# Kernel tuning notes

Measured on AMD Instinct MI355X. Metric: run time of the kernel, lower is better.

Reference implementation:

```python
import jax, jax.numpy as jnp
import numpy as np

B, N, C = 4, 2048, 1024
H, D = 16, 64  # num_heads, head_dim; C = H*D
R = 16         # lora rank
SCALE = D ** -0.5


def setup_inputs() -> dict:
    key = jax.random.key(0)
    ks = jax.random.split(key, 6)
    return {
        "query": jax.random.normal(ks[0], (B, N, C), dtype=jnp.float32),
        "mask": jax.random.normal(ks[1], (B, 1, N, N), dtype=jnp.float32),
        "W_qkv": jax.random.normal(ks[2], (C, 3 * C), dtype=jnp.float32) * (C ** -0.5),
        "magnitude": jnp.ones((1, H, 1, 1), dtype=jnp.float32),
        "W_loraA": jax.random.normal(ks[3], (C, R), dtype=jnp.float32) * (C ** -0.5),
        "W_loraB": jax.random.normal(ks[4], (R, C), dtype=jnp.float32) * (R ** -0.5),
        "W_proj": jax.random.normal(ks[5], (C, C), dtype=jnp.float32) * (C ** -0.5),
    }


def reference(query, mask, W_qkv, magnitude, W_loraA, W_loraB, W_proj):
    # qkv projection: [B,N,3C] -> [3,B,H,N,D]
    qkv = (query @ W_qkv).reshape(B, N, 3, H, D).transpose(2, 0, 3, 1, 4)
    q, k, v = qkv[0], qkv[1], qkv[2]
    # LoRA/DoRA delta fused into q before attention
    delta = (query @ W_loraA) @ W_loraB                     # [B,N,C]
    delta = delta.reshape(B, N, H, D).transpose(0, 2, 1, 3)  # [B,H,N,D]
    q = q + magnitude * delta
    # attention
    attn = jnp.einsum('bhnd,bhmd->bhnm', q, k) * SCALE + mask
    attn = jax.nn.softmax(attn, axis=-1)
    out = jnp.einsum('bhnm,bhmd->bhnd', attn, v)            # [B,H,N,D]
    out = out.transpose(0, 2, 1, 3).reshape(B, N, C)
    return out @ W_proj
```

## Files before the change

kernel.cpp:

```cpp
#include <hip/hip_runtime.h>
#include <hip/hip_bf16.h>

#define Bd 4
#define Nd 2048
#define Cd 1024
#define Hd 16
#define Dd 64
#define Rd 16
#define KAUG 1056
#define SCALEf 0.125f
#define PIT 72

using short8 = __attribute__((ext_vector_type(8))) short;
using f32x4  = __attribute__((ext_vector_type(4))) float;

static __device__ __forceinline__ ushort f2bf(float f) {
    __hip_bfloat16 h = __float2bfloat16(f);
    return *reinterpret_cast<ushort*>(&h);
}

#define GLOAD_LDS16(g, l) __builtin_amdgcn_global_load_lds( \
    (const __attribute__((address_space(1))) void*)(g),      \
    (__attribute__((address_space(3))) void*)(l), 16, 0, 0)

__global__ __launch_bounds__(256) void pack_a_kernel(
    const float* __restrict__ query, ushort* __restrict__ Aaug)
{
    const int row = blockIdx.x;
    const int t = threadIdx.x;
    const float4 v = *(const float4*)&query[(size_t)row * Cd + t * 4];
    ushort4 u;
    u.x = f2bf(v.x); u.y = f2bf(v.y); u.z = f2bf(v.z); u.w = f2bf(v.w);
    *(ushort4*)&Aaug[(size_t)row * KAUG + t * 4] = u;
}

__global__ __launch_bounds__(256) void pack_wat_kernel(
    const float* __restrict__ WA, ushort* __restrict__ WAT)
{
    const int idx = blockIdx.x * 256 + threadIdx.x;
    const int c = idx >> 4, r = idx & 15;
    WAT[r * 1024 + c] = f2bf(WA[idx]);
}

__global__ __launch_bounds__(64) void lora_mfma_kernel(
    const ushort* __restrict__ Aro, const ushort* __restrict__ WAT,
    ushort* __restrict__ Awr)
{
    const int lane = threadIdx.x;
    const int quad = lane >> 4, lc = lane & 15;
    const int row0 = blockIdx.x * 16;
    f32x4 acc = {0.f, 0.f, 0.f, 0.f};
    #pragma unroll 4
    for (int k0 = 0; k0 < 1024; k0 += 32) {
        const short8 a = *(const short8*)&Aro[(size_t)(row0 + lc) * KAUG + k0 + quad * 8];
        const short8 b = *(const short8*)&WAT[lc * 1024 + k0 + quad * 8];
        acc = __builtin_amdgcn_mfma_f32_16x16x32_bf16(a, b, acc, 0, 0, 0);
    }
    #pragma unroll
    for (int ri = 0; ri < 4; ++ri) {
        const size_t row = row0 + quad * 4 + ri;
        Awr[row * KAUG + 1024 + lc] = f2bf(acc[ri]);
        Awr[row * KAUG + 1040 + lc] = 0;
    }
}

__global__ __launch_bounds__(256) void pack_bqkv_kernel(
    const float* __restrict__ Wqkv, const float* __restrict__ WloraB,
    const float* __restrict__ magnitude, ushort* __restrict__ BT)
{
    __shared__ float tile[32][33];
    const int k0 = blockIdx.x * 32, n0 = blockIdx.y * 32;
    const int tx = threadIdx.x & 31, ty = threadIdx.x >> 5;
    #pragma unroll
    for (int i = 0; i < 4; ++i) {
        const int k = k0 + ty + i * 8;
        const int n = n0 + tx;
        float v;
        if (k < 1024)                      v = Wqkv[(size_t)k * 3072 + n];
        else if (k < 1040 && n < 1024)     v = magnitude[n >> 6] * WloraB[(k - 1024) * Cd + n];
        else                               v = 0.f;
        tile[ty + i * 8][tx] = v;
    }
    __syncthreads();
    #pragma unroll
    for (int i = 0; i < 4; ++i) {
        const int n = n0 + ty + i * 8;
        const int k = k0 + tx;
        BT[(size_t)n * KAUG + k] = f2bf(tile[tx][ty + i * 8]);
    }
}

__global__ __launch_bounds__(256) void pack_bproj_kernel(
    const float* __restrict__ Wp, ushort* __restrict__ BT)
{
    __shared__ float tile[32][33];
    const int k0 = blockIdx.x * 32, n0 = blockIdx.y * 32;
    const int tx = threadIdx.x & 31, ty = threadIdx.x >> 5;
    #pragma unroll
    for (int i = 0; i < 4; ++i)
        tile[ty + i * 8][tx] = Wp[(size_t)(k0 + ty + i * 8) * Cd + n0 + tx];
    __syncthreads();
    #pragma unroll
    for (int i = 0; i < 4; ++i)
        BT[(size_t)(n0 + ty + i * 8) * Cd + k0 + tx] = f2bf(tile[tx][ty + i * 8]);
}

template <int KD, int MODE>
__global__ __launch_bounds__(256) void mfma_gemm_kernel(
    const ushort* __restrict__ Ag, const ushort* __restrict__ Bg,
    ushort* __restrict__ qb, ushort* __restrict__ kb, ushort* __restrict__ vb,
    float* __restrict__ outf)
{
    __shared__ ushort As[128 * 32];
    __shared__ ushort Bs[128 * 32];
    const int t = threadIdx.x;
    const int w = t >> 6, lane = t & 63, quad = lane >> 4, lc = lane & 15;
    const int wm = w >> 1, wn = w & 1;
    const int m0 = blockIdx.y * 128, n0 = blockIdx.x * 128;

    f32x4 acc[4][4] = {};

    const int lin0 = t, lin1 = t + 256;
    const int rowT0 = lin0 >> 2, kc0 = (lin0 & 3) * 8;
    const int rowT1 = lin1 >> 2, kc1 = (lin1 & 3) * 8;

    for (int k0 = 0; k0 < KD; k0 += 32) {
        GLOAD_LDS16(&Ag[(size_t)(m0 + rowT0) * KD + k0 + kc0], &As[lin0 * 8]);
        GLOAD_LDS16(&Ag[(size_t)(m0 + rowT1) * KD + k0 + kc1], &As[lin1 * 8]);
        GLOAD_LDS16(&Bg[(size_t)(n0 + rowT0) * KD + k0 + kc0], &Bs[lin0 * 8]);
        GLOAD_LDS16(&Bg[(size_t)(n0 + rowT1) * KD + k0 + kc1], &Bs[lin1 * 8]);
        __syncthreads();
        short8 a[4], b[4];
        #pragma unroll
        for (int i = 0; i < 4; ++i)
            a[i] = *(const short8*)&As[(wm * 64 + i * 16 + lc) * 32 + quad * 8];
        #pragma unroll
        for (int j = 0; j < 4; ++j)
            b[j] = *(const short8*)&Bs[(wn * 64 + j * 16 + lc) * 32 + quad * 8];
        #pragma unroll
        for (int i = 0; i < 4; ++i)
            #pragma unroll
            for (int j = 0; j < 4; ++j)
                acc[i][j] = __builtin_amdgcn_mfma_f32_16x16x32_bf16(a[i], b[j], acc[i][j], 0, 0, 0);
        __syncthreads();
    }

    if (MODE == 0) {
        const int sec = n0 >> 10;
        ushort* dst = sec == 0 ? qb : (sec == 1 ? kb : vb);
        #pragma unroll
        for (int i = 0; i < 4; ++i)
            #pragma unroll
            for (int j = 0; j < 4; ++j) {
                const int gcol = (n0 & 1023) + wn * 64 + j * 16 + lc;
                const int h = gcol >> 6, d = gcol & 63;
                #pragma unroll
                for (int r = 0; r < 4; ++r) {
                    const int grow = m0 + wm * 64 + i * 16 + quad * 4 + r;
                    const int b_ = grow >> 11, n_ = grow & 2047;
                    dst[(((size_t)(b_ * Hd) + h) * Nd + n_) * Dd + d] = f2bf(acc[i][j][r]);
                }
            }
    } else {
        #pragma unroll
        for (int i = 0; i < 4; ++i)
            #pragma unroll
            for (int j = 0; j < 4; ++j) {
                const int gcol = n0 + wn * 64 + j * 16 + lc;
                #pragma unroll
                for (int r = 0; r < 4; ++r) {
                    const int grow = m0 + wm * 64 + i * 16 + quad * 4 + r;
                    outf[(size_t)grow * Cd + gcol] = acc[i][j][r];
                }
            }
    }
}

__global__ __launch_bounds__(256) void attn_mfma_kernel(
    const ushort* __restrict__ qbuf, const ushort* __restrict__ kbuf,
    const ushort* __restrict__ vbuf, const float* __restrict__ mask,
    ushort* __restrict__ attn_out)
{
    __shared__ short Ks[64 * PIT];
    __shared__ short Vts[64 * PIT];
    __shared__ short Ps[128 * PIT];

    const int t = threadIdx.x;
    const int w = t >> 6, lane = t & 63;
    const int quad = lane >> 4, lc = lane & 15;
    const int bh = blockIdx.y, b = bh >> 4, h = bh & 15;
    const int n0 = blockIdx.x * 128;

    const short* qg = (const short*)qbuf + (size_t)bh * Nd * Dd;
    const short* kg = (const short*)kbuf + (size_t)bh * Nd * Dd;
    const short* vg = (const short*)vbuf + (size_t)bh * Nd * Dd;
    const float* mbase = mask + ((size_t)b * Nd + n0) * Nd;

    short8 qf[2][2];
    #pragma unroll
    for (int sub = 0; sub < 2; ++sub)
        #pragma unroll
        for (int ks = 0; ks < 2; ++ks)
            qf[sub][ks] = *(const short8*)
                &qg[(size_t)(n0 + w * 32 + sub * 16 + lc) * Dd + ks * 32 + quad * 8];

    float rs[2][4];
    f32x4 o[2][4];
    #pragma unroll
    for (int sub = 0; sub < 2; ++sub)
        #pragma unroll
        for (int dt = 0; dt < 4; ++dt) {
            o[sub][dt] = (f32x4){0.f, 0.f, 0.f, 0.f};
            rs[sub][dt] = 0.f;
        }

    for (int m0 = 0; m0 < Nd; m0 += 64) {
        {
            const int row = t >> 2, dblk = (t & 3) * 16;
            *(int4*)&Ks[row * PIT + dblk]     = *(const int4*)&kg[(m0 + row) * Dd + dblk];
            *(int4*)&Ks[row * PIT + dblk + 8] = *(const int4*)&kg[(m0 + row) * Dd + dblk + 8];
        }
        {
            const int kv0 = (t >> 3) * 2;
            const int dg = t & 7, d0 = dg * 8;
            ushort u0[8], u1[8];
            *(int4*)u0 = *(const int4*)&vg[(m0 + kv0) * Dd + d0];
            *(int4*)u1 = *(const int4*)&vg[(m0 + kv0 + 1) * Dd + d0];
            const int blk = ((kv0 >> 3) ^ dg) & 7;
            #pragma unroll
            for (int i = 0; i < 8; ++i) {
                *(uint*)&Vts[(d0 + i) * PIT + blk * 8 + (kv0 & 7)] =
                    (uint)u0[i] | ((uint)u1[i] << 16);
            }
        }
        float mk0[4][4];
        #pragma unroll
        for (int r = 0; r < 4; ++r)
            #pragma unroll
            for (int nt = 0; nt < 4; ++nt)
                mk0[r][nt] = mbase[(size_t)(w * 32 + quad * 4 + r) * Nd
                                   + m0 + nt * 16 + lc];
        __syncthreads();

        f32x4 s[2][4];
        #pragma unroll
        for (int sub = 0; sub < 2; ++sub)
            #pragma unroll
            for (int nt = 0; nt < 4; ++nt)
                s[sub][nt] = (f32x4){0.f, 0.f, 0.f, 0.f};
        #pragma unroll
        for (int ks = 0; ks < 2; ++ks)
            #pragma unroll
            for (int nt = 0; nt < 4; ++nt) {
                const short8 kf = *(const short8*)
                    &Ks[(nt * 16 + lc) * PIT + ks * 32 + quad * 8];
                s[0][nt] = __builtin_amdgcn_mfma_f32_16x16x32_bf16(qf[0][ks], kf, s[0][nt], 0, 0, 0);
                s[1][nt] = __builtin_amdgcn_mfma_f32_16x16x32_bf16(qf[1][ks], kf, s[1][nt], 0, 0, 0);
            }

        float mk1[4][4];
        #pragma unroll
        for (int r = 0; r < 4; ++r)
            #pragma unroll
            for (int nt = 0; nt < 4; ++nt)
                mk1[r][nt] = mbase[(size_t)(w * 32 + 16 + quad * 4 + r) * Nd
                                   + m0 + nt * 16 + lc];

        {
            const int rowg = w * 32 + quad * 4;
            #pragma unroll
            for (int nt = 0; nt < 4; ++nt) {
                const int cbx = ((nt * 2 + (lc >> 3)) ^ quad) * 8 + (lc & 7);
                const float p0 = __expf(fmaf(s[0][nt][0], SCALEf, mk0[0][nt]));
                const float p1 = __expf(fmaf(s[0][nt][1], SCALEf, mk0[1][nt]));
                const float p2 = __expf(fmaf(s[0][nt][2], SCALEf, mk0[2][nt]));
                const float p3 = __expf(fmaf(s[0][nt][3], SCALEf, mk0[3][nt]));
                rs[0][0] += p0; rs[0][1] += p1; rs[0][2] += p2; rs[0][3] += p3;
                uint pk01, pk23;
                asm("v_cvt_pk_bf16_f32 %0, %1, %2" : "=v"(pk01) : "v"(p0), "v"(p1));
                asm("v_cvt_pk_bf16_f32 %0, %1, %2" : "=v"(pk23) : "v"(p2), "v"(p3));
                Ps[(rowg + 0) * PIT + cbx] = (short)pk01;
                Ps[(rowg + 1) * PIT + cbx] = (short)(pk01 >> 16);
                Ps[(rowg + 2) * PIT + cbx] = (short)pk23;
                Ps[(rowg + 3) * PIT + cbx] = (short)(pk23 >> 16);
            }
        }
        {
            const int rowg = w * 32 + 16 + quad * 4;
            #pragma unroll
            for (int nt = 0; nt < 4; ++nt) {
                const int cbx = ((nt * 2 + (lc >> 3)) ^ quad) * 8 + (lc & 7);
                const float p0 = __expf(fmaf(s[1][nt][0], SCALEf, mk1[0][nt]));
                const float p1 = __expf(fmaf(s[1][nt][1], SCALEf, mk1[1][nt]));
                const float p2 = __expf(fmaf(s[1][nt][2], SCALEf, mk1[2][nt]));
                const float p3 = __expf(fmaf(s[1][nt][3], SCALEf, mk1[3][nt]));
                rs[1][0] += p0; rs[1][1] += p1; rs[1][2] += p2; rs[1][3] += p3;
                uint pk01, pk23;
                asm("v_cvt_pk_bf16_f32 %0, %1, %2" : "=v"(pk01) : "v"(p0), "v"(p1));
                asm("v_cvt_pk_bf16_f32 %0, %1, %2" : "=v"(pk23) : "v"(p2), "v"(p3));
                Ps[(rowg + 0) * PIT + cbx] = (short)pk01;
                Ps[(rowg + 1) * PIT + cbx] = (short)(pk01 >> 16);
                Ps[(rowg + 2) * PIT + cbx] = (short)pk23;
                Ps[(rowg + 3) * PIT + cbx] = (short)(pk23 >> 16);
            }
        }
        #pragma unroll
        for (int ks = 0; ks < 2; ++ks) {
            short8 bb[4];
            #pragma unroll
            for (int dt = 0; dt < 4; ++dt) {
                const int d = dt * 16 + lc;
                const int blk = (ks * 4 + quad) ^ ((d >> 3) & 7);
                bb[dt] = *(const short8*)&Vts[d * PIT + blk * 8];
            }
            const int pblk = (((ks * 4 + quad) ^ ((lc >> 2) & 3)) & 7) * 8;
            #pragma unroll
            for (int sub = 0; sub < 2; ++sub) {
                const short8 a = *(const short8*)&Ps[(w * 32 + sub * 16 + lc) * PIT + pblk];
                #pragma unroll
                for (int dt = 0; dt < 4; ++dt)
                    o[sub][dt] = __builtin_amdgcn_mfma_f32_16x16x32_bf16(a, bb[dt], o[sub][dt], 0, 0, 0);
            }
        }
        __syncthreads();
    }

    #pragma unroll
    for (int sub = 0; sub < 2; ++sub) {
        const int rowg = w * 32 + sub * 16 + quad * 4;
        #pragma unroll
        for (int r = 0; r < 4; ++r) {
            float v = rs[sub][r];
            v += __shfl_xor(v, 1);
            v += __shfl_xor(v, 2);
            v += __shfl_xor(v, 4);
            v += __shfl_xor(v, 8);
            const float inv = 1.f / v;
            const size_t rowo = ((size_t)(b * Nd + n0 + rowg + r)) * Cd + h * Dd;
            #pragma unroll
            for (int dt = 0; dt < 4; ++dt)
                attn_out[rowo + dt * 16 + lc] = f2bf(o[sub][dt][r] * inv);
        }
    }
}

extern "C" void kernel_launch(void* const* d_in, const int* in_sizes, int n_in,
                              void* d_out, int out_size, void* d_ws, size_t ws_size,
                              hipStream_t stream) {
    const float* query     = (const float*)d_in[0];
    const float* mask      = (const float*)d_in[1];
    const float* Wqkv      = (const float*)d_in[2];
    const float* magnitude = (const float*)d_in[3];
    const float* WloraA    = (const float*)d_in[4];
    const float* WloraB    = (const float*)d_in[5];
    const float* Wproj     = (const float*)d_in[6];
    float* out = (float*)d_out;

    const size_t SZ = (size_t)Bd * Hd * Nd * Dd;
    char* p = (char*)d_ws;
    ushort* qbuf = (ushort*)p;           p += SZ * 2;
    ushort* kbuf = (ushort*)p;           p += SZ * 2;
    ushort* vbuf = (ushort*)p;           p += SZ * 2;
    ushort* aout = (ushort*)p;           p += SZ * 2;
    ushort* Aaug = (ushort*)p;           p += (size_t)8192 * KAUG * 2;
    ushort* BT   = (ushort*)p;           p += (size_t)3072 * KAUG * 2;
    ushort* WpT  = (ushort*)p;           p += (size_t)1024 * 1024 * 2;
    ushort* WAT  = (ushort*)p;           p += (size_t)16 * 1024 * 2;

    pack_a_kernel<<<dim3(Bd * Nd), 256, 0, stream>>>(query, Aaug);
    pack_wat_kernel<<<dim3(64), 256, 0, stream>>>(WloraA, WAT);
    pack_bqkv_kernel<<<dim3(KAUG / 32, 3072 / 32), 256, 0, stream>>>(
        Wqkv, WloraB, magnitude, BT);
    pack_bproj_kernel<<<dim3(32, 32), 256, 0, stream>>>(Wproj, WpT);
    lora_mfma_kernel<<<dim3(512), 64, 0, stream>>>(Aaug, WAT, Aaug);
    mfma_gemm_kernel<KAUG, 0><<<dim3(24, 64), 256, 0, stream>>>(
        Aaug, BT, qbuf, kbuf, vbuf, nullptr);
    attn_mfma_kernel<<<dim3(Nd / 128, Bd * Hd), 256, 0, stream>>>(
        qbuf, kbuf, vbuf, mask, aout);
    mfma_gemm_kernel<1024, 1><<<dim3(8, 64), 256, 0, stream>>>(
        aout, WpT, nullptr, nullptr, nullptr, out);
}
```

Measured before the change: 422.7 us.

## Prefetch next K/V tiles into registers to overlap global loads with MFMA

The attention loop now loads the following 64-row K and V tiles from global memory into registers while the current tile is being computed. Ks is refilled right after the QK^T MFMAs and Vts right after the PV MFMAs. Barriers are moved so each LDS buffer is rewritten only once all waves have finished reading it. The aim is to hide global-load latency behind compute, at the cost of more live registers, which may reduce occupancy, and one redundant wrapped-around prefetch at the end of the loop.

```diff
diff --git a/kernel.cpp b/kernel.cpp
--- a/kernel.cpp
+++ b/kernel.cpp
@@ -214,25 +214,32 @@
             rs[sub][dt] = 0.f;
         }
 
+    const int krow = t >> 2, kcol = (t & 3) * 16;
+    const int kv0 = (t >> 3) * 2, dgv = t & 7, d0v = dgv * 8;
+    const int vblk = ((kv0 >> 3) ^ dgv) & 7;
+
+    int4 kr0, kr1, vr0, vr1;
+    kr0 = *(const int4*)&kg[(size_t)krow * Dd + kcol];
+    kr1 = *(const int4*)&kg[(size_t)krow * Dd + kcol + 8];
+    vr0 = *(const int4*)&vg[(size_t)kv0 * Dd + d0v];
+    vr1 = *(const int4*)&vg[(size_t)(kv0 + 1) * Dd + d0v];
+    *(int4*)&Ks[krow * PIT + kcol]     = kr0;
+    *(int4*)&Ks[krow * PIT + kcol + 8] = kr1;
+    {
+        ushort u0[8], u1[8];
+        *(int4*)u0 = vr0; *(int4*)u1 = vr1;
+        #pragma unroll
+        for (int i = 0; i < 8; ++i)
+            *(uint*)&Vts[(d0v + i) * PIT + vblk * 8 + (kv0 & 7)] =
+                (uint)u0[i] | ((uint)u1[i] << 16);
+    }
+    kr0 = *(const int4*)&kg[(size_t)(64 + krow) * Dd + kcol];
+    kr1 = *(const int4*)&kg[(size_t)(64 + krow) * Dd + kcol + 8];
+    vr0 = *(const int4*)&vg[(size_t)(64 + kv0) * Dd + d0v];
+    vr1 = *(const int4*)&vg[(size_t)(64 + kv0 + 1) * Dd + d0v];
+    __syncthreads();
+
     for (int m0 = 0; m0 < Nd; m0 += 64) {
-        {
-            const int row = t >> 2, dblk = (t & 3) * 16;
-            *(int4*)&Ks[row * PIT + dblk]     = *(const int4*)&kg[(m0 + row) * Dd + dblk];
-            *(int4*)&Ks[row * PIT + dblk + 8] = *(const int4*)&kg[(m0 + row) * Dd + dblk + 8];
-        }
-        {
-            const int kv0 = (t >> 3) * 2;
-            const int dg = t & 7, d0 = dg * 8;
-            ushort u0[8], u1[8];
-            *(int4*)u0 = *(const int4*)&vg[(m0 + kv0) * Dd + d0];
-            *(int4*)u1 = *(const int4*)&vg[(m0 + kv0 + 1) * Dd + d0];
-            const int blk = ((kv0 >> 3) ^ dg) & 7;
-            #pragma unroll
-            for (int i = 0; i < 8; ++i) {
-                *(uint*)&Vts[(d0 + i) * PIT + blk * 8 + (kv0 & 7)] =
-                    (uint)u0[i] | ((uint)u1[i] << 16);
-            }
-        }
         float mk0[4][4];
         #pragma unroll
         for (int r = 0; r < 4; ++r)
@@ -240,7 +247,6 @@
             for (int nt = 0; nt < 4; ++nt)
                 mk0[r][nt] = mbase[(size_t)(w * 32 + quad * 4 + r) * Nd
                                    + m0 + nt * 16 + lc];
-        __syncthreads();
 
         f32x4 s[2][4];
         #pragma unroll
@@ -257,6 +263,13 @@
                 s[0][nt] = __builtin_amdgcn_mfma_f32_16x16x32_bf16(qf[0][ks], kf, s[0][nt], 0, 0, 0);
                 s[1][nt] = __builtin_amdgcn_mfma_f32_16x16x32_bf16(qf[1][ks], kf, s[1][nt], 0, 0, 0);
             }
+        __syncthreads();
+
+        *(int4*)&Ks[krow * PIT + kcol]     = kr0;
+        *(int4*)&Ks[krow * PIT + kcol + 8] = kr1;
+        const int mnx = (m0 + 128) & (Nd - 1);
+        kr0 = *(const int4*)&kg[(size_t)(mnx + krow) * Dd + kcol];
+        kr1 = *(const int4*)&kg[(size_t)(mnx + krow) * Dd + kcol + 8];
 
         float mk1[4][4];
         #pragma unroll
@@ -323,6 +336,17 @@
             }
         }
         __syncthreads();
+
+        {
+            ushort u0[8], u1[8];
+            *(int4*)u0 = vr0; *(int4*)u1 = vr1;
+            #pragma unroll
+            for (int i = 0; i < 8; ++i)
+                *(uint*)&Vts[(d0v + i) * PIT + vblk * 8 + (kv0 & 7)] =
+                    (uint)u0[i] | ((uint)u1[i] << 16);
+        }
+        vr0 = *(const int4*)&vg[(size_t)(mnx + kv0) * Dd + d0v];
+        vr1 = *(const int4*)&vg[(size_t)(mnx + kv0 + 1) * Dd + d0v];
     }
 
     #pragma unroll
```

After: 405.6 us. 1.04x faster.
